# Kernel tuning notes

Hardware: AMD Instinct MI355X
Metric: run time of the kernel (lower is better)

The kernel has to match this reference:

```python
import jax, jax.numpy as jnp
import numpy as np

B, C, H, W = 2, 192, 96, 96
HEADS, DG, KH, KW = 12, 12, 3, 3
K = KH * KW
PAD, DIL = KH // 2, 1
MLP_HIDDEN = 2 * C  # mlp_ratio = 2


def setup_inputs() -> dict:
    key = jax.random.key(0)
    ks = jax.random.split(key, 14)
    s = 0.02
    return {
        "q": jax.random.normal(ks[0], (B, C, H, W), jnp.float32),
        "k": jax.random.normal(ks[1], (B, C, H, W), jnp.float32),
        "v": jax.random.normal(ks[2], (B, C, H, W), jnp.float32),
        "offset": jax.random.normal(ks[3], (B, DG * 2 * K, H, W), jnp.float32),
        "Wq": jax.random.normal(ks[4], (C, C), jnp.float32) * s,
        "bq": jax.random.normal(ks[5], (C,), jnp.float32) * s,
        "Wk": jax.random.normal(ks[6], (C, C), jnp.float32) * s,
        "bk": jax.random.normal(ks[7], (C,), jnp.float32) * s,
        "Wv": jax.random.normal(ks[8], (C, C), jnp.float32) * s,
        "bv": jax.random.normal(ks[9], (C,), jnp.float32) * s,
        "W1": jax.random.normal(ks[10], (C, MLP_HIDDEN), jnp.float32) * s,
        "b1": jax.random.normal(ks[11], (MLP_HIDDEN,), jnp.float32) * s,
        "W2": jax.random.normal(ks[12], (MLP_HIDDEN, C), jnp.float32) * s,
        "b2": jax.random.normal(ks[13], (C,), jnp.float32) * s,
    }


def _bilinear_sample(img, py, px):
    """img: [B,G,Cg,H,W]; py,px: [B,G,K,H,W] fractional sample coords.
    Returns [B,G,Cg,K,H,W]; zero outside image (DCN-style per-corner masking)."""
    b, g, cg, h, w = img.shape
    y0 = jnp.floor(py)
    x0 = jnp.floor(px)
    wy1 = py - y0
    wx1 = px - x0
    wy0 = 1.0 - wy1
    wx0 = 1.0 - wx1
    imgf = img.reshape(b, g, cg, h * w)

    def corner(yi, xi, wgt):
        valid = ((yi >= 0) & (yi <= h - 1) & (xi >= 0) & (xi <= w - 1)).astype(img.dtype)
        yc = jnp.clip(yi, 0, h - 1).astype(jnp.int32)
        xc = jnp.clip(xi, 0, w - 1).astype(jnp.int32)
        idx = (yc * w + xc).reshape(b, g, 1, -1)  # [B,G,1,K*H*W]
        gth = jnp.take_along_axis(imgf, idx, axis=3)  # [B,G,Cg,K*H*W]
        return gth * (valid * wgt).reshape(b, g, 1, -1)

    out = (corner(y0, x0, wy0 * wx0)
           + corner(y0, x0 + 1, wy0 * wx1)
           + corner(y0 + 1, x0, wy1 * wx0)
           + corner(y0 + 1, x0 + 1, wy1 * wx1))
    return out.reshape(b, g, cg, py.shape[2], h, w)


def _forward(q, k, v, offset, Wq, bq, Wk, bk, Wv, bv, W1, b1, W2, b2):
    def lin(x, Wm, bb):  # per-pixel Linear over channel dim
        return jnp.einsum('bchw,cd->bdhw', x, Wm) + bb[None, :, None, None]

    qp = lin(q, Wq, bq)
    kp = lin(k, Wk, bk)
    vp = lin(v, Wv, bv)

    # DCN-v1 offset layout: [B, G, K, 2(y,x), H, W]
    off = offset.reshape(B, DG, K, 2, H, W)
    ii, jj = jnp.meshgrid(jnp.arange(KH), jnp.arange(KW), indexing='ij')
    ii = ii.reshape(K)
    jj = jj.reshape(K)
    base_y = (jnp.arange(H)[None, :] - PAD + (ii * DIL)[:, None]).astype(jnp.float32)  # [K,H]
    base_x = (jnp.arange(W)[None, :] - PAD + (jj * DIL)[:, None]).astype(jnp.float32)  # [K,W]
    py = base_y[None, None, :, :, None] + off[:, :, :, 0]  # [B,G,K,H,W]
    px = base_x[None, None, :, None, :] + off[:, :, :, 1]

    cg = C // DG
    k_s = _bilinear_sample(kp.reshape(B, DG, cg, H, W), py, px)  # [B,G,cg,K,H,W]
    v_s = _bilinear_sample(vp.reshape(B, DG, cg, H, W), py, px)

    hd = C // HEADS
    k_s = k_s.reshape(B, HEADS, hd, K, H, W)
    v_s = v_s.reshape(B, HEADS, hd, K, H, W)
    qh = qp.reshape(B, HEADS, hd, H, W)

    scale = hd ** -0.5
    scores = jnp.einsum('bndhw,bndkhw->bnkhw', qh, k_s) * scale
    attn = jax.nn.softmax(scores, axis=2)  # over K sampled points (clip_size=1)
    out = jnp.einsum('bnkhw,bndkhw->bndhw', attn, v_s).reshape(B, C, H, W)

    # residual MLP (GELU exact, as torch nn.GELU default)
    xf = out.transpose(0, 2, 3, 1)  # [B,H,W,C]
    h1 = jax.nn.gelu(xf @ W1 + b1, approximate=False)
    mlp = (h1 @ W2 + b2).transpose(0, 3, 1, 2)
    return out + mlp


def reference(q, k, v, offset, Wq, bq, Wk, bk, Wv, bv, W1, b1, W2, b2):
    return _forward(q, k, v, offset, Wq, bq, Wk, bk, Wv, bv, W1, b1, W2, b2)
```

## Files before the change

### kernel.cpp

```cpp
#include <hip/hip_runtime.h>
#include <hip/hip_bf16.h>
#include <math.h>

#define B_    2
#define C_    192
#define H_    96
#define W_    96
#define HW_   (H_ * W_)
#define NPIX_ (B_ * HW_)
#define G_    12
#define CG_   16
#define KPTS_ 9
#define MLPH_ 384
#define OFFCH (G_ * 2 * KPTS_)

typedef __attribute__((ext_vector_type(8))) short s16x8;
typedef __attribute__((ext_vector_type(4))) float f32x4;

__device__ __forceinline__ ushort f2b(float f) {
    __hip_bfloat16 h = __float2bfloat16(f);
    return *reinterpret_cast<ushort*>(&h);
}
__device__ __forceinline__ float b2f(ushort u) {
    return __uint_as_float(((uint)u) << 16);
}
__device__ __forceinline__ float b2f_lo(uint u) { return __uint_as_float(u << 16); }
__device__ __forceinline__ float b2f_hi(uint u) { return __uint_as_float(u & 0xffff0000u); }

#if __has_builtin(__builtin_amdgcn_fdot2_f32_bf16)
typedef __attribute__((ext_vector_type(2))) __bf16 bf16x2;
#define HAVE_DOT2BF 1
__device__ __forceinline__ float dot2bf(uint a, uint b, float c) {
    return __builtin_amdgcn_fdot2_f32_bf16(__builtin_bit_cast(bf16x2, a),
                                           __builtin_bit_cast(bf16x2, b), c, false);
}
#else
#define HAVE_DOT2BF 0
#endif

#define GLOAD16(gp, lp)                                                          \
    __builtin_amdgcn_global_load_lds(                                            \
        (const __attribute__((address_space(1))) void*)(gp),                     \
        (__attribute__((address_space(3))) void*)(lp), 16, 0, 0)

__global__ __launch_bounds__(256) void prep_kernel(
    const float* __restrict__ q, const float* __restrict__ k,
    const float* __restrict__ v, const float* __restrict__ offset,
    const float* __restrict__ Wq, const float* __restrict__ Wk,
    const float* __restrict__ Wv, const float* __restrict__ W1,
    const float* __restrict__ W2,
    ushort* __restrict__ Xcl, float* __restrict__ offT, ushort* __restrict__ Wt)
{
    __shared__ ushort sm[64][196];
    const int bx = blockIdx.x;
    const int t  = threadIdx.x;

    if (bx < 864) {
        const int z   = bx / 288;
        const int rem = bx - z * 288;
        const int b   = rem / 144;
        const int hw0 = (rem - b * 144) * 64;
        const float* X = (z == 0) ? q : (z == 1) ? k : v;

        const int hwl = t & 63;
        #pragma unroll 4
        for (int j = 0; j < 48; ++j) {
            const int c = (t >> 6) + j * 4;
            sm[hwl][c] = f2b(X[(b * C_ + c) * HW_ + hw0 + hwl]);
        }
        __syncthreads();
        #pragma unroll
        for (int jj = 0; jj < 12; ++jj) {
            const int idx = t + 256 * jj;
            const int row = idx / 48, cq = idx - row * 48;
            const int pix = b * HW_ + hw0 + row;
            *(uint2*)&Xcl[((z * NPIX_) + pix) * C_ + cq * 4] = *(uint2*)&sm[row][cq * 4];
        }
    } else if (bx < 1152) {
        const int rem = bx - 864;
        const int b   = rem / 144;
        const int hw0 = (rem - b * 144) * 64;
        #pragma unroll
        for (int j = 0; j < 54; ++j) {
            const int i = t + 256 * j;
            const int pixl = i / OFFCH, p = i - pixl * OFFCH;
            offT[(size_t)(b * HW_ + hw0 + pixl) * OFFCH + p] =
                offset[(size_t)(b * OFFCH + p) * HW_ + hw0 + pixl];
        }
    } else {
        const int i = (bx - 1152) * 256 + t;
        if (i < 110592) {
            const int s = i / 36864, j = i - s * 36864;
            const float* src = (s == 0) ? Wq : (s == 1) ? Wk : Wv;
            const int d = j / 192, c = j - d * 192;
            Wt[i] = f2b(src[c * 192 + d]);
        } else if (i < 184320) {
            const int j = i - 110592, d = j / 192, c = j - d * 192;
            Wt[i] = f2b(W1[c * 384 + d]);
        } else if (i < 258048) {
            const int j = i - 184320, d = j / 384, c = j - d * 384;
            Wt[i] = f2b(W2[c * 192 + d]);
        }
    }
}

template<int KK>
__device__ __forceinline__ void stage_tiles64(const ushort* Az, const ushort* Bz,
                                              ushort* dst, int t, int m0, int n0, int kt)
{
    #pragma unroll
    for (int j = 0; j < 4; ++j) {
        const int qq = t + 256 * j;
        const int r = qq >> 3, p = qq & 7;
        const int s = p ^ (r & 7);
        GLOAD16(Az + (size_t)(m0 + r) * KK + kt * 64 + s * 8, dst + qq * 8);
    }
    #pragma unroll
    for (int j = 0; j < 2; ++j) {
        const int qq = t + 256 * j;
        const int r = qq >> 3, p = qq & 7;
        const int s = p ^ (r & 7);
        GLOAD16(Bz + (size_t)(n0 + r) * KK + kt * 64 + s * 8, dst + 8192 + qq * 8);
    }
}

template<int KK, int EPI>
__global__ __launch_bounds__(256) void gemm_kernel(
    const ushort* __restrict__ A,  const ushort* __restrict__ BT,
    const float* __restrict__ bias0, const float* __restrict__ bias1,
    const float* __restrict__ bias2,
    ushort* __restrict__ Ob, ushort* __restrict__ Okv,
    const ushort* __restrict__ res, float* __restrict__ Onchw,
    int zAstr, int zBstr)
{
    __shared__ char lds_raw[49152];
    ushort* smem = (ushort*)lds_raw;

    const int t  = threadIdx.x;
    const int l  = t & 63;
    const int wid = t >> 6;
    const int wm = wid >> 1, wn = wid & 1;
    const int m0 = blockIdx.x * 128;
    const int n0 = blockIdx.y * 64;
    const int z  = blockIdx.z;
    const int Ntot = gridDim.y * 64;
    constexpr int NKT = KK / 64;

    const ushort* Az = A  + (size_t)z * zAstr;
    const ushort* Bz = BT + (size_t)z * zBstr;
    const float* bias = (z == 0) ? bias0 : (z == 1) ? bias1 : bias2;

    int aoff[4][2], boff[2][2];
    #pragma unroll
    for (int f = 0; f < 4; ++f) {
        const int r = wm * 64 + f * 16 + (l & 15);
        #pragma unroll
        for (int ks = 0; ks < 2; ++ks) {
            const int c = ks * 4 + (l >> 4);
            aoff[f][ks] = r * 64 + (c ^ (r & 7)) * 8;
        }
    }
    #pragma unroll
    for (int g = 0; g < 2; ++g) {
        const int r = wn * 32 + g * 16 + (l & 15);
        #pragma unroll
        for (int ks = 0; ks < 2; ++ks) {
            const int c = ks * 4 + (l >> 4);
            boff[g][ks] = 8192 + r * 64 + (c ^ (r & 7)) * 8;
        }
    }

    f32x4 acc[4][2] = {};

    stage_tiles64<KK>(Az, Bz, smem, t, m0, n0, 0);
    __syncthreads();

    for (int kt = 0; kt < NKT; ++kt) {
        if (kt + 1 < NKT)
            stage_tiles64<KK>(Az, Bz, smem + ((kt + 1) & 1) * 12288, t, m0, n0, kt + 1);

        const ushort* buf = smem + (kt & 1) * 12288;
        s16x8 af[4][2], bf[2][2];
        #pragma unroll
        for (int f = 0; f < 4; ++f)
            #pragma unroll
            for (int ks = 0; ks < 2; ++ks) af[f][ks] = *(const s16x8*)(buf + aoff[f][ks]);
        #pragma unroll
        for (int g = 0; g < 2; ++g)
            #pragma unroll
            for (int ks = 0; ks < 2; ++ks) bf[g][ks] = *(const s16x8*)(buf + boff[g][ks]);
        #pragma unroll
        for (int ks = 0; ks < 2; ++ks)
            #pragma unroll
            for (int f = 0; f < 4; ++f)
                #pragma unroll
                for (int g = 0; g < 2; ++g)
                    acc[f][g] = __builtin_amdgcn_mfma_f32_16x16x32_bf16(af[f][ks], bf[g][ks], acc[f][g], 0, 0, 0);
        __syncthreads();
    }

    const int rowg = l >> 4, ncol = l & 15;
    float bv[2];
    #pragma unroll
    for (int g = 0; g < 2; ++g) bv[g] = bias[n0 + wn * 32 + g * 16 + ncol];

    if constexpr (EPI == 0) {
        if (z == 0) {
            #pragma unroll
            for (int f = 0; f < 4; ++f)
                #pragma unroll
                for (int g = 0; g < 2; ++g)
                    #pragma unroll
                    for (int r = 0; r < 4; ++r) {
                        const int m = m0 + wm * 64 + f * 16 + rowg * 4 + r;
                        const int n = n0 + wn * 32 + g * 16 + ncol;
                        Ob[(size_t)m * C_ + n] = f2b(acc[f][g][r] + bv[g]);
                    }
        } else {
            const int voff = (z == 2) ? 16 : 0;
            #pragma unroll
            for (int f = 0; f < 4; ++f)
                #pragma unroll
                for (int g = 0; g < 2; ++g) {
                    const int grp = (n0 >> 4) + wn * 2 + g;
                    #pragma unroll
                    for (int r = 0; r < 4; ++r) {
                        const int m = m0 + wm * 64 + f * 16 + rowg * 4 + r;
                        Okv[(size_t)m * (2 * C_) + grp * 32 + voff + ncol] =
                            f2b(acc[f][g][r] + bv[g]);
                    }
                }
        }
    } else if constexpr (EPI == 1) {
        #pragma unroll
        for (int f = 0; f < 4; ++f)
            #pragma unroll
            for (int g = 0; g < 2; ++g)
                #pragma unroll
                for (int r = 0; r < 4; ++r) {
                    const int m = m0 + wm * 64 + f * 16 + rowg * 4 + r;
                    const int n = n0 + wn * 32 + g * 16 + ncol;
                    const float x = acc[f][g][r] + bv[g];
                    Ob[(size_t)m * Ntot + n] = f2b(0.5f * x * (1.f + erff(x * 0.70710678118f)));
                }
    } else {
        float* tsp = (float*)lds_raw;
        #pragma unroll
        for (int f = 0; f < 4; ++f)
            #pragma unroll
            for (int g = 0; g < 2; ++g)
                #pragma unroll
                for (int r = 0; r < 4; ++r) {
                    const int ml = wm * 64 + f * 16 + rowg * 4 + r;
                    const int nl = wn * 32 + g * 16 + ncol;
                    const float rv = b2f(res[(size_t)(m0 + ml) * C_ + n0 + nl]);
                    tsp[nl * 132 + ml] = acc[f][g][r] + bv[g] + rv;
                }
        __syncthreads();
        const int b   = m0 / HW_;
        const int hw0 = m0 - b * HW_;
        #pragma unroll
        for (int jj = 0; jj < 8; ++jj) {
            const int i4 = t + 256 * jj;
            const int nn = i4 >> 5, mc = i4 & 31;
            float4 val = *(float4*)&tsp[nn * 132 + mc * 4];
            *(float4*)&Onchw[(size_t)b * C_ * HW_ + (size_t)(n0 + nn) * HW_ + hw0 + mc * 4] = val;
        }
    }
}

__global__ __launch_bounds__(256, 2) void deform_attn_kernel(
    const ushort* __restrict__ qb, const ushort* __restrict__ kvb,
    const float* __restrict__ offT, ushort* __restrict__ aob)
{
    const int t   = threadIdx.x;
    const int bid = blockIdx.x;
    const int xb  = (bid & 7) * 432 + (bid >> 3);
    const int pair = xb * 64 + (t >> 2);
    const int lane4 = t & 3;
    const int g   = pair % G_;
    const int pix = pair / G_;
    const int b   = pix / HW_;
    const int hw  = pix - b * HW_;
    const int h   = hw / W_;
    const int w   = hw - h * W_;
    const int gc0 = g * CG_ + lane4 * 4;

    uint2 qu = *(const uint2*)(qb + (size_t)pix * C_ + gc0);

    const float* ob_ = offT + (size_t)pix * OFFCH + g * (2 * KPTS_);
    float offy[3] = {0.f, 0.f, 0.f}, offx[3] = {0.f, 0.f, 0.f};
    {
        float2 p0 = *(const float2*)(ob_ + lane4 * 2);
        float2 p1 = *(const float2*)(ob_ + (lane4 + 4) * 2);
        offy[0] = p0.x; offx[0] = p0.y;
        offy[1] = p1.x; offx[1] = p1.y;
        if (lane4 == 0) {
            float2 p2 = *(const float2*)(ob_ + 16);
            offy[2] = p2.x; offx[2] = p2.y;
        }
    }

    int   addr[KPTS_][4];
    float wgt[KPTS_][4];
    #pragma unroll
    for (int kk = 0; kk < KPTS_; ++kk) {
        const float oy = __shfl(offy[kk >> 2], kk & 3, 4);
        const float ox = __shfl(offx[kk >> 2], kk & 3, 4);
        const float py = (float)(h - 1 + kk / 3) + oy;
        const float px = (float)(w - 1 + kk % 3) + ox;
        const float fy = floorf(py), fx = floorf(px);
        const int   y0 = (int)fy,   x0 = (int)fx;
        const float wy1 = py - fy, wx1 = px - fx;
        const float wy0 = 1.f - wy1, wx0 = 1.f - wx1;

        const float wy0m = ((unsigned)y0       < (unsigned)H_) ? wy0 : 0.f;
        const float wy1m = ((unsigned)(y0 + 1) < (unsigned)H_) ? wy1 : 0.f;
        const float wx0m = ((unsigned)x0       < (unsigned)W_) ? wx0 : 0.f;
        const float wx1m = ((unsigned)(x0 + 1) < (unsigned)W_) ? wx1 : 0.f;
        const int yc0 = min(max(y0, 0), H_ - 1);
        const int yc1 = min(max(y0 + 1, 0), H_ - 1);
        const int xc0 = min(max(x0, 0), W_ - 1);
        const int xc1 = min(max(x0 + 1, 0), W_ - 1);

        const int kvbase = g * 32 + lane4 * 4;
        addr[kk][0] = ((b * HW_ + yc0 * W_ + xc0) * (2 * C_)) + kvbase;  wgt[kk][0] = wy0m * wx0m;
        addr[kk][1] = ((b * HW_ + yc0 * W_ + xc1) * (2 * C_)) + kvbase;  wgt[kk][1] = wy0m * wx1m;
        addr[kk][2] = ((b * HW_ + yc1 * W_ + xc0) * (2 * C_)) + kvbase;  wgt[kk][2] = wy1m * wx0m;
        addr[kk][3] = ((b * HW_ + yc1 * W_ + xc1) * (2 * C_)) + kvbase;  wgt[kk][3] = wy1m * wx1m;
    }

    float score[KPTS_];
    uint2 vu[KPTS_][4];
    #pragma unroll
    for (int kk = 0; kk < KPTS_; ++kk) {
        float s = 0.f;
        #pragma unroll
        for (int c = 0; c < 4; ++c) {
            const uint2 ku = *(const uint2*)(kvb + addr[kk][c]);
            vu[kk][c]      = *(const uint2*)(kvb + addr[kk][c] + 16);
#if HAVE_DOT2BF
            const float d = dot2bf(ku.y, qu.y, dot2bf(ku.x, qu.x, 0.f));
#else
            float d = b2f_lo(qu.x) * b2f_lo(ku.x);
            d = fmaf(b2f_hi(qu.x), b2f_hi(ku.x), d);
            d = fmaf(b2f_lo(qu.y), b2f_lo(ku.y), d);
            d = fmaf(b2f_hi(qu.y), b2f_hi(ku.y), d);
#endif
            s = fmaf(wgt[kk][c], d, s);
        }
        score[kk] = s;
    }
    #pragma unroll
    for (int kk = 0; kk < KPTS_; ++kk) {
        float sc = score[kk];
        sc += __shfl_xor(sc, 1, 4);
        sc += __shfl_xor(sc, 2, 4);
        score[kk] = sc * 0.25f;
    }

    float m = score[0];
    #pragma unroll
    for (int kk = 1; kk < KPTS_; ++kk) m = fmaxf(m, score[kk]);
    float ssum = 0.f;
    #pragma unroll
    for (int kk = 0; kk < KPTS_; ++kk) { score[kk] = __expf(score[kk] - m); ssum += score[kk]; }
    const float inv = 1.f / ssum;

    f32x4 o = {0.f, 0.f, 0.f, 0.f};
    #pragma unroll
    for (int kk = 0; kk < KPTS_; ++kk) {
        const float p = score[kk] * inv;
        #pragma unroll
        for (int c = 0; c < 4; ++c) {
            const float pw = p * wgt[kk][c];
            o[0] = fmaf(pw, b2f_lo(vu[kk][c].x), o[0]);
            o[1] = fmaf(pw, b2f_hi(vu[kk][c].x), o[1]);
            o[2] = fmaf(pw, b2f_lo(vu[kk][c].y), o[2]);
            o[3] = fmaf(pw, b2f_hi(vu[kk][c].y), o[3]);
        }
    }

    uint2 obv;
    obv.x = (uint)f2b(o[0]) | ((uint)f2b(o[1]) << 16);
    obv.y = (uint)f2b(o[2]) | ((uint)f2b(o[3]) << 16);
    *(uint2*)(aob + (size_t)pix * C_ + gc0) = obv;
}

extern "C" void kernel_launch(void* const* d_in, const int* in_sizes, int n_in,
                              void* d_out, int out_size, void* d_ws, size_t ws_size,
                              hipStream_t stream)
{
    const float* q      = (const float*)d_in[0];
    const float* k      = (const float*)d_in[1];
    const float* v      = (const float*)d_in[2];
    const float* offset = (const float*)d_in[3];
    const float* Wq     = (const float*)d_in[4];
    const float* bq     = (const float*)d_in[5];
    const float* Wk     = (const float*)d_in[6];
    const float* bk     = (const float*)d_in[7];
    const float* Wv     = (const float*)d_in[8];
    const float* bv     = (const float*)d_in[9];
    const float* W1     = (const float*)d_in[10];
    const float* b1     = (const float*)d_in[11];
    const float* W2     = (const float*)d_in[12];
    const float* b2     = (const float*)d_in[13];

    ushort* ws0 = (ushort*)d_ws;
    ushort* Xcl = ws0;
    ushort* aob = Xcl;
    ushort* qb  = Xcl + (size_t)3 * NPIX_ * C_;
    ushort* kvb = qb  + (size_t)NPIX_ * C_;
    ushort* Hb  = kvb + (size_t)NPIX_ * 2 * C_;
    ushort* Wt  = Hb  + (size_t)NPIX_ * MLPH_;
    ushort* W1T = Wt + 110592;
    ushort* W2T = Wt + 184320;
    float*  offT = (float*)(Wt + 258048);

    prep_kernel<<<2160, 256, 0, stream>>>(q, k, v, offset, Wq, Wk, Wv, W1, W2,
                                          Xcl, offT, Wt);

    gemm_kernel<192, 0><<<dim3(NPIX_ / 128, 3, 3), 256, 0, stream>>>(
        Xcl, Wt, bq, bk, bv, qb, kvb, nullptr, nullptr,
        NPIX_ * C_, C_ * C_);

    deform_attn_kernel<<<NPIX_ * G_ / 64, 256, 0, stream>>>(qb, kvb, offT, aob);

    gemm_kernel<192, 1><<<dim3(NPIX_ / 128, 6, 1), 256, 0, stream>>>(
        aob, W1T, b1, b1, b1, Hb, nullptr, nullptr, nullptr, 0, 0);

    gemm_kernel<384, 2><<<dim3(NPIX_ / 128, 3, 1), 256, 0, stream>>>(
        Hb, W2T, b2, b2, b2, nullptr, nullptr, aob, (float*)d_out, 0, 0);
}
```

Measured before the change: 208.0 us.

## Fuse MLP GEMMs, drop offset transpose, single-stage projection GEMM, slimmer deform attention

```diff
diff --git a/kernel.cpp b/kernel.cpp
--- a/kernel.cpp
+++ b/kernel.cpp
@@ -43,13 +43,17 @@
         (const __attribute__((address_space(1))) void*)(gp),                     \
         (__attribute__((address_space(3))) void*)(lp), 16, 0, 0)
 
+__device__ __forceinline__ int swz(int c, int r) {
+    return (c & ~7) | ((c & 7) ^ (r & 7));
+}
+
 __global__ __launch_bounds__(256) void prep_kernel(
     const float* __restrict__ q, const float* __restrict__ k,
-    const float* __restrict__ v, const float* __restrict__ offset,
+    const float* __restrict__ v,
     const float* __restrict__ Wq, const float* __restrict__ Wk,
     const float* __restrict__ Wv, const float* __restrict__ W1,
     const float* __restrict__ W2,
-    ushort* __restrict__ Xcl, float* __restrict__ offT, ushort* __restrict__ Wt)
+    ushort* __restrict__ Xcl, ushort* __restrict__ Wt)
 {
     __shared__ ushort sm[64][196];
     const int bx = blockIdx.x;
@@ -76,19 +80,8 @@
             const int pix = b * HW_ + hw0 + row;
             *(uint2*)&Xcl[((z * NPIX_) + pix) * C_ + cq * 4] = *(uint2*)&sm[row][cq * 4];
         }
-    } else if (bx < 1152) {
-        const int rem = bx - 864;
-        const int b   = rem / 144;
-        const int hw0 = (rem - b * 144) * 64;
-        #pragma unroll
-        for (int j = 0; j < 54; ++j) {
-            const int i = t + 256 * j;
-            const int pixl = i / OFFCH, p = i - pixl * OFFCH;
-            offT[(size_t)(b * HW_ + hw0 + pixl) * OFFCH + p] =
-                offset[(size_t)(b * OFFCH + p) * HW_ + hw0 + pixl];
-        }
     } else {
-        const int i = (bx - 1152) * 256 + t;
+        const int i = (bx - 864) * 256 + t;
         if (i < 110592) {
             const int s = i / 36864, j = i - s * 36864;
             const float* src = (s == 0) ? Wq : (s == 1) ? Wk : Wv;
@@ -104,37 +97,15 @@
     }
 }
 
-template<int KK>
-__device__ __forceinline__ void stage_tiles64(const ushort* Az, const ushort* Bz,
-                                              ushort* dst, int t, int m0, int n0, int kt)
+__global__ __launch_bounds__(256) void proj_kernel(
+    const ushort* __restrict__ A, const ushort* __restrict__ Wt,
+    const float* __restrict__ bq, const float* __restrict__ bk,
+    const float* __restrict__ bv,
+    ushort* __restrict__ qb, ushort* __restrict__ kvb)
 {
-    #pragma unroll
-    for (int j = 0; j < 4; ++j) {
-        const int qq = t + 256 * j;
-        const int r = qq >> 3, p = qq & 7;
-        const int s = p ^ (r & 7);
-        GLOAD16(Az + (size_t)(m0 + r) * KK + kt * 64 + s * 8, dst + qq * 8);
-    }
-    #pragma unroll
-    for (int j = 0; j < 2; ++j) {
-        const int qq = t + 256 * j;
-        const int r = qq >> 3, p = qq & 7;
-        const int s = p ^ (r & 7);
-        GLOAD16(Bz + (size_t)(n0 + r) * KK + kt * 64 + s * 8, dst + 8192 + qq * 8);
-    }
-}
-
-template<int KK, int EPI>
-__global__ __launch_bounds__(256) void gemm_kernel(
-    const ushort* __restrict__ A,  const ushort* __restrict__ BT,
-    const float* __restrict__ bias0, const float* __restrict__ bias1,
-    const float* __restrict__ bias2,
-    ushort* __restrict__ Ob, ushort* __restrict__ Okv,
-    const ushort* __restrict__ res, float* __restrict__ Onchw,
-    int zAstr, int zBstr)
-{
-    __shared__ char lds_raw[49152];
-    ushort* smem = (ushort*)lds_raw;
+    __shared__ char lds[73728];
+    ushort* As = (ushort*)lds;
+    ushort* Bs = (ushort*)lds + 24576;
 
     const int t  = threadIdx.x;
     const int l  = t & 63;
@@ -143,135 +114,83 @@
     const int m0 = blockIdx.x * 128;
     const int n0 = blockIdx.y * 64;
     const int z  = blockIdx.z;
-    const int Ntot = gridDim.y * 64;
-    constexpr int NKT = KK / 64;
-
-    const ushort* Az = A  + (size_t)z * zAstr;
-    const ushort* Bz = BT + (size_t)z * zBstr;
-    const float* bias = (z == 0) ? bias0 : (z == 1) ? bias1 : bias2;
-
-    int aoff[4][2], boff[2][2];
-    #pragma unroll
-    for (int f = 0; f < 4; ++f) {
-        const int r = wm * 64 + f * 16 + (l & 15);
-        #pragma unroll
-        for (int ks = 0; ks < 2; ++ks) {
-            const int c = ks * 4 + (l >> 4);
-            aoff[f][ks] = r * 64 + (c ^ (r & 7)) * 8;
-        }
-    }
-    #pragma unroll
-    for (int g = 0; g < 2; ++g) {
-        const int r = wn * 32 + g * 16 + (l & 15);
-        #pragma unroll
-        for (int ks = 0; ks < 2; ++ks) {
-            const int c = ks * 4 + (l >> 4);
-            boff[g][ks] = 8192 + r * 64 + (c ^ (r & 7)) * 8;
-        }
-    }
-
+
+    const ushort* Az = A  + (size_t)z * NPIX_ * C_;
+    const ushort* Bz = Wt + (size_t)z * C_ * C_;
+    const float* bias = (z == 0) ? bq : (z == 1) ? bk : bv;
+
+    #pragma unroll
+    for (int j = 0; j < 12; ++j) {
+        const int qq = t + 256 * j;
+        const int r = qq / 24, cc = qq - r * 24;
+        GLOAD16(Az + (size_t)(m0 + r) * C_ + swz(cc, r) * 8, As + qq * 8);
+    }
+    #pragma unroll
+    for (int j = 0; j < 6; ++j) {
+        const int qq = t + 256 * j;
+        const int r = qq / 24, cc = qq - r * 24;
+        GLOAD16(Bz + (size_t)(n0 + r) * C_ + swz(cc, r) * 8, Bs + qq * 8);
+    }
+    __syncthreads();
+
+    const int lr = l & 15, lq = l >> 4;
     f32x4 acc[4][2] = {};
-
-    stage_tiles64<KK>(Az, Bz, smem, t, m0, n0, 0);
-    __syncthreads();
-
-    for (int kt = 0; kt < NKT; ++kt) {
-        if (kt + 1 < NKT)
-            stage_tiles64<KK>(Az, Bz, smem + ((kt + 1) & 1) * 12288, t, m0, n0, kt + 1);
-
-        const ushort* buf = smem + (kt & 1) * 12288;
-        s16x8 af[4][2], bf[2][2];
-        #pragma unroll
-        for (int f = 0; f < 4; ++f)
-            #pragma unroll
-            for (int ks = 0; ks < 2; ++ks) af[f][ks] = *(const s16x8*)(buf + aoff[f][ks]);
-        #pragma unroll
-        for (int g = 0; g < 2; ++g)
-            #pragma unroll
-            for (int ks = 0; ks < 2; ++ks) bf[g][ks] = *(const s16x8*)(buf + boff[g][ks]);
-        #pragma unroll
-        for (int ks = 0; ks < 2; ++ks)
-            #pragma unroll
-            for (int f = 0; f < 4; ++f)
-                #pragma unroll
-                for (int g = 0; g < 2; ++g)
-                    acc[f][g] = __builtin_amdgcn_mfma_f32_16x16x32_bf16(af[f][ks], bf[g][ks], acc[f][g], 0, 0, 0);
-        __syncthreads();
-    }
-
-    const int rowg = l >> 4, ncol = l & 15;
-    float bv[2];
-    #pragma unroll
-    for (int g = 0; g < 2; ++g) bv[g] = bias[n0 + wn * 32 + g * 16 + ncol];
-
-    if constexpr (EPI == 0) {
-        if (z == 0) {
-            #pragma unroll
-            for (int f = 0; f < 4; ++f)
-                #pragma unroll
-                for (int g = 0; g < 2; ++g)
-                    #pragma unroll
-                    for (int r = 0; r < 4; ++r) {
-                        const int m = m0 + wm * 64 + f * 16 + rowg * 4 + r;
-                        const int n = n0 + wn * 32 + g * 16 + ncol;
-                        Ob[(size_t)m * C_ + n] = f2b(acc[f][g][r] + bv[g]);
-                    }
-        } else {
-            const int voff = (z == 2) ? 16 : 0;
-            #pragma unroll
-            for (int f = 0; f < 4; ++f)
-                #pragma unroll
-                for (int g = 0; g < 2; ++g) {
-                    const int grp = (n0 >> 4) + wn * 2 + g;
-                    #pragma unroll
-                    for (int r = 0; r < 4; ++r) {
-                        const int m = m0 + wm * 64 + f * 16 + rowg * 4 + r;
-                        Okv[(size_t)m * (2 * C_) + grp * 32 + voff + ncol] =
-                            f2b(acc[f][g][r] + bv[g]);
-                    }
-                }
-        }
-    } else if constexpr (EPI == 1) {
+    #pragma unroll
+    for (int ks = 0; ks < 6; ++ks) {
+        const int c = ks * 4 + lq;
+        s16x8 af[4], bf[2];
+        #pragma unroll
+        for (int f = 0; f < 4; ++f) {
+            const int r = wm * 64 + f * 16 + lr;
+            af[f] = *(const s16x8*)(As + r * 192 + swz(c, r) * 8);
+        }
+        #pragma unroll
+        for (int g = 0; g < 2; ++g) {
+            const int r = wn * 32 + g * 16 + lr;
+            bf[g] = *(const s16x8*)(Bs + r * 192 + swz(c, r) * 8);
+        }
+        #pragma unroll
+        for (int f = 0; f < 4; ++f)
+            #pragma unroll
+            for (int g = 0; g < 2; ++g)
+                acc[f][g] = __builtin_amdgcn_mfma_f32_16x16x32_bf16(af[f], bf[g], acc[f][g], 0, 0, 0);
+    }
+
+    float bvv[2];
+    #pragma unroll
+    for (int g = 0; g < 2; ++g) bvv[g] = bias[n0 + wn * 32 + g * 16 + lr];
+
+    if (z == 0) {
         #pragma unroll
         for (int f = 0; f < 4; ++f)
             #pragma unroll
             for (int g = 0; g < 2; ++g)
                 #pragma unroll
                 for (int r = 0; r < 4; ++r) {
-                    const int m = m0 + wm * 64 + f * 16 + rowg * 4 + r;
-                    const int n = n0 + wn * 32 + g * 16 + ncol;
-                    const float x = acc[f][g][r] + bv[g];
-                    Ob[(size_t)m * Ntot + n] = f2b(0.5f * x * (1.f + erff(x * 0.70710678118f)));
+                    const int m = m0 + wm * 64 + f * 16 + lq * 4 + r;
+                    const int n = n0 + wn * 32 + g * 16 + lr;
+                    qb[(size_t)m * C_ + n] = f2b(acc[f][g][r] + bvv[g]);
                 }
     } else {
-        float* tsp = (float*)lds_raw;
-        #pragma unroll
-        for (int f = 0; f < 4; ++f)
-            #pragma unroll
-            for (int g = 0; g < 2; ++g)
+        const int voff = (z == 2) ? 16 : 0;
+        #pragma unroll
+        for (int f = 0; f < 4; ++f)
+            #pragma unroll
+            for (int g = 0; g < 2; ++g) {
+                const int grp = (n0 >> 4) + wn * 2 + g;
                 #pragma unroll
                 for (int r = 0; r < 4; ++r) {
-                    const int ml = wm * 64 + f * 16 + rowg * 4 + r;
-                    const int nl = wn * 32 + g * 16 + ncol;
-                    const float rv = b2f(res[(size_t)(m0 + ml) * C_ + n0 + nl]);
-                    tsp[nl * 132 + ml] = acc[f][g][r] + bv[g] + rv;
+                    const int m = m0 + wm * 64 + f * 16 + lq * 4 + r;
+                    kvb[(size_t)m * (2 * C_) + grp * 32 + voff + lr] =
+                        f2b(acc[f][g][r] + bvv[g]);
                 }
-        __syncthreads();
-        const int b   = m0 / HW_;
-        const int hw0 = m0 - b * HW_;
-        #pragma unroll
-        for (int jj = 0; jj < 8; ++jj) {
-            const int i4 = t + 256 * jj;
-            const int nn = i4 >> 5, mc = i4 & 31;
-            float4 val = *(float4*)&tsp[nn * 132 + mc * 4];
-            *(float4*)&Onchw[(size_t)b * C_ * HW_ + (size_t)(n0 + nn) * HW_ + hw0 + mc * 4] = val;
-        }
-    }
-}
-
-__global__ __launch_bounds__(256, 2) void deform_attn_kernel(
+            }
+    }
+}
+
+__global__ __launch_bounds__(256, 4) void deform_attn_kernel(
     const ushort* __restrict__ qb, const ushort* __restrict__ kvb,
-    const float* __restrict__ offT, ushort* __restrict__ aob)
+    const float* __restrict__ offset, ushort* __restrict__ aob)
 {
     const int t   = threadIdx.x;
     const int bid = blockIdx.x;
@@ -288,16 +207,16 @@
 
     uint2 qu = *(const uint2*)(qb + (size_t)pix * C_ + gc0);
 
-    const float* ob_ = offT + (size_t)pix * OFFCH + g * (2 * KPTS_);
     float offy[3] = {0.f, 0.f, 0.f}, offx[3] = {0.f, 0.f, 0.f};
     {
-        float2 p0 = *(const float2*)(ob_ + lane4 * 2);
-        float2 p1 = *(const float2*)(ob_ + (lane4 + 4) * 2);
-        offy[0] = p0.x; offx[0] = p0.y;
-        offy[1] = p1.x; offx[1] = p1.y;
-        if (lane4 == 0) {
-            float2 p2 = *(const float2*)(ob_ + 16);
-            offy[2] = p2.x; offx[2] = p2.y;
+        const int obase = (b * OFFCH + g * (2 * KPTS_)) * HW_ + hw;
+        #pragma unroll
+        for (int s = 0; s < 3; ++s) {
+            const int kk = lane4 + s * 4;
+            if (kk < KPTS_) {
+                offy[s] = offset[obase + (kk * 2) * HW_];
+                offx[s] = offset[obase + (kk * 2 + 1) * HW_];
+            }
         }
     }
 
@@ -331,14 +250,12 @@
     }
 
     float score[KPTS_];
-    uint2 vu[KPTS_][4];
     #pragma unroll
     for (int kk = 0; kk < KPTS_; ++kk) {
         float s = 0.f;
         #pragma unroll
         for (int c = 0; c < 4; ++c) {
             const uint2 ku = *(const uint2*)(kvb + addr[kk][c]);
-            vu[kk][c]      = *(const uint2*)(kvb + addr[kk][c] + 16);
 #if HAVE_DOT2BF
             const float d = dot2bf(ku.y, qu.y, dot2bf(ku.x, qu.x, 0.f));
 #else
@@ -370,21 +287,140 @@
     f32x4 o = {0.f, 0.f, 0.f, 0.f};
     #pragma unroll
     for (int kk = 0; kk < KPTS_; ++kk) {
-        const float p = score[kk] * inv;
+        const float p = score[kk];
         #pragma unroll
         for (int c = 0; c < 4; ++c) {
             const float pw = p * wgt[kk][c];
-            o[0] = fmaf(pw, b2f_lo(vu[kk][c].x), o[0]);
-            o[1] = fmaf(pw, b2f_hi(vu[kk][c].x), o[1]);
-            o[2] = fmaf(pw, b2f_lo(vu[kk][c].y), o[2]);
-            o[3] = fmaf(pw, b2f_hi(vu[kk][c].y), o[3]);
+            const uint2 vv = *(const uint2*)(kvb + addr[kk][c] + 16);
+            o[0] = fmaf(pw, b2f_lo(vv.x), o[0]);
+            o[1] = fmaf(pw, b2f_hi(vv.x), o[1]);
+            o[2] = fmaf(pw, b2f_lo(vv.y), o[2]);
+            o[3] = fmaf(pw, b2f_hi(vv.y), o[3]);
         }
     }
 
     uint2 obv;
-    obv.x = (uint)f2b(o[0]) | ((uint)f2b(o[1]) << 16);
-    obv.y = (uint)f2b(o[2]) | ((uint)f2b(o[3]) << 16);
+    obv.x = (uint)f2b(o[0] * inv) | ((uint)f2b(o[1] * inv) << 16);
+    obv.y = (uint)f2b(o[2] * inv) | ((uint)f2b(o[3] * inv) << 16);
     *(uint2*)(aob + (size_t)pix * C_ + gc0) = obv;
+}
+
+__global__ __launch_bounds__(256) void mlp_fused_kernel(
+    const ushort* __restrict__ aob, const ushort* __restrict__ W1T,
+    const ushort* __restrict__ W2T, const float* __restrict__ b1,
+    const float* __restrict__ b2, float* __restrict__ out)
+{
+    __shared__ char lds[73728];
+    ushort* As = (ushort*)lds;
+    ushort* Hs = (ushort*)lds + 12288;
+
+    const int t = threadIdx.x;
+    const int l = t & 63;
+    const int w = t >> 6;
+    const int pix0 = blockIdx.x * 64;
+    const int lr = l & 15, lq = l >> 4;
+
+    #pragma unroll
+    for (int j = 0; j < 6; ++j) {
+        const int qq = t + 256 * j;
+        const int r = qq / 24, cc = qq - r * 24;
+        GLOAD16(aob + (size_t)(pix0 + r) * C_ + swz(cc, r) * 8, As + qq * 8);
+    }
+    __syncthreads();
+
+    const int n0w = w * 96;
+    f32x4 acc1[4][6] = {};
+    #pragma unroll
+    for (int ks = 0; ks < 6; ++ks) {
+        const int c = ks * 4 + lq;
+        s16x8 af[4], bf[6];
+        #pragma unroll
+        for (int f = 0; f < 4; ++f) {
+            const int r = f * 16 + lr;
+            af[f] = *(const s16x8*)(As + r * 192 + swz(c, r) * 8);
+        }
+        #pragma unroll
+        for (int g = 0; g < 6; ++g)
+            bf[g] = *(const s16x8*)(W1T + (size_t)(n0w + g * 16 + lr) * C_ + ks * 32 + lq * 8);
+        #pragma unroll
+        for (int f = 0; f < 4; ++f)
+            #pragma unroll
+            for (int g = 0; g < 6; ++g)
+                acc1[f][g] = __builtin_amdgcn_mfma_f32_16x16x32_bf16(af[f], bf[g], acc1[f][g], 0, 0, 0);
+    }
+    #pragma unroll
+    for (int g = 0; g < 6; ++g) {
+        const int n = n0w + g * 16 + lr;
+        const float bb = b1[n];
+        const int c = n >> 3, nlo = n & 7;
+        #pragma unroll
+        for (int f = 0; f < 4; ++f)
+            #pragma unroll
+            for (int r = 0; r < 4; ++r) {
+                const int m = f * 16 + lq * 4 + r;
+                const float x = acc1[f][g][r] + bb;
+                Hs[m * 384 + swz(c, m) * 8 + nlo] =
+                    f2b(0.5f * x * (1.f + erff(x * 0.70710678118f)));
+            }
+    }
+    __syncthreads();
+
+    const int n0w2 = w * 48;
+    f32x4 acc2[4][3] = {};
+    #pragma unroll
+    for (int ks = 0; ks < 12; ++ks) {
+        const int c = ks * 4 + lq;
+        s16x8 af[4], bf[3];
+        #pragma unroll
+        for (int f = 0; f < 4; ++f) {
+            const int r = f * 16 + lr;
+            af[f] = *(const s16x8*)(Hs + r * 384 + swz(c, r) * 8);
+        }
+        #pragma unroll
+        for (int g = 0; g < 3; ++g)
+            bf[g] = *(const s16x8*)(W2T + (size_t)(n0w2 + g * 16 + lr) * MLPH_ + ks * 32 + lq * 8);
+        #pragma unroll
+        for (int f = 0; f < 4; ++f)
+            #pragma unroll
+            for (int g = 0; g < 3; ++g)
+                acc2[f][g] = __builtin_amdgcn_mfma_f32_16x16x32_bf16(af[f], bf[g], acc2[f][g], 0, 0, 0);
+    }
+    #pragma unroll
+    for (int g = 0; g < 3; ++g) {
+        const int n = n0w2 + g * 16 + lr;
+        const float bb = b2[n];
+        const int c = n >> 3, nlo = n & 7;
+        #pragma unroll
+        for (int f = 0; f < 4; ++f)
+            #pragma unroll
+            for (int r = 0; r < 4; ++r) {
+                const int m = f * 16 + lq * 4 + r;
+                acc2[f][g][r] += bb + b2f(As[m * 192 + swz(c, m) * 8 + nlo]);
+            }
+    }
+    __syncthreads();
+    float* tsp = (float*)lds;
+    #pragma unroll
+    for (int g = 0; g < 3; ++g) {
+        const int n = n0w2 + g * 16 + lr;
+        #pragma unroll
+        for (int f = 0; f < 4; ++f)
+            #pragma unroll
+            for (int r = 0; r < 4; ++r) {
+                const int m = f * 16 + lq * 4 + r;
+                tsp[n * 68 + m] = acc2[f][g][r];
+            }
+    }
+    __syncthreads();
+    const int b   = pix0 / HW_;
+    const int hw0 = pix0 - b * HW_;
+    #pragma unroll
+    for (int j = 0; j < 12; ++j) {
+        const int i = t + 256 * j;
+        const int nn = i >> 4, mc = i & 15;
+        float4 val = *(float4*)&tsp[nn * 68 + mc * 4];
+        *(float4*)&out[(size_t)(b * C_ + nn) * HW_ + hw0 + mc * 4] = val;
+    }
 }
 
 extern "C" void kernel_launch(void* const* d_in, const int* in_sizes, int n_in,
@@ -406,29 +442,21 @@
     const float* W2     = (const float*)d_in[12];
     const float* b2     = (const float*)d_in[13];
 
-    ushort* ws0 = (ushort*)d_ws;
-    ushort* Xcl = ws0;
+    ushort* Xcl = (ushort*)d_ws;
     ushort* aob = Xcl;
     ushort* qb  = Xcl + (size_t)3 * NPIX_ * C_;
     ushort* kvb = qb  + (size_t)NPIX_ * C_;
-    ushort* Hb  = kvb + (size_t)NPIX_ * 2 * C_;
-    ushort* Wt  = Hb  + (size_t)NPIX_ * MLPH_;
+    ushort* Wt  = kvb + (size_t)NPIX_ * 2 * C_;
     ushort* W1T = Wt + 110592;
     ushort* W2T = Wt + 184320;
-    float*  offT = (float*)(Wt + 258048);
-
-    prep_kernel<<<2160, 256, 0, stream>>>(q, k, v, offset, Wq, Wk, Wv, W1, W2,
-                                          Xcl, offT, Wt);
-
-    gemm_kernel<192, 0><<<dim3(NPIX_ / 128, 3, 3), 256, 0, stream>>>(
-        Xcl, Wt, bq, bk, bv, qb, kvb, nullptr, nullptr,
-        NPIX_ * C_, C_ * C_);
-
-    deform_attn_kernel<<<NPIX_ * G_ / 64, 256, 0, stream>>>(qb, kvb, offT, aob);
-
-    gemm_kernel<192, 1><<<dim3(NPIX_ / 128, 6, 1), 256, 0, stream>>>(
-        aob, W1T, b1, b1, b1, Hb, nullptr, nullptr, nullptr, 0, 0);
-
-    gemm_kernel<384, 2><<<dim3(NPIX_ / 128, 3, 1), 256, 0, stream>>>(
-        Hb, W2T, b2, b2, b2, nullptr, nullptr, aob, (float*)d_out, 0, 0);
-}
+
+    prep_kernel<<<1872, 256, 0, stream>>>(q, k, v, Wq, Wk, Wv, W1, W2, Xcl, Wt);
+
+    proj_kernel<<<dim3(NPIX_ / 128, 3, 3), 256, 0, stream>>>(
+        Xcl, Wt, bq, bk, bv, qb, kvb);
+
+    deform_attn_kernel<<<NPIX_ * G_ / 64, 256, 0, stream>>>(qb, kvb, offset, aob);
+
+    mlp_fused_kernel<<<NPIX_ / 64, 256, 0, stream>>>(
+        aob, W1T, W2T, b1, b2, (float*)d_out);
+}
```

Result: slower. 259.8 us (+24.9%).
